# Optimization experiments

Hardware: AMD Instinct MI355X
Metric: run time of the kernel (lower is better)

Reference implementation:

```python
import math
import jax, jax.numpy as jnp
import numpy as np

T_MIN = 0.1
T_MAX = 1.0


def _log_cond_prob(energy, text_mask, mel_mask, direction, neg):
    # energy: (B, I, J); returns (B, I, J, K) with K=J (alpha) or J-1 (beta)
    B, I, J = energy.shape
    if direction == 'alpha':
        K = J
        tri_jk = jnp.arange(J)[:, None] >= jnp.arange(K)[None, :]  # torch triu: valid if j >= k
    else:
        K = J - 1
        tri_jk = jnp.arange(J)[:, None] <= jnp.arange(K)[None, :]  # torch tril: valid if j <= k
    tm = text_mask[:, :, None, None]           # (B,I,1,1)
    mmj = mel_mask[:, None, :, None]           # (B,1,J,1)
    mmk = mel_mask[:, None, None, :K]          # (B,1,1,K)
    mask = tm & mmj & mmk                      # (B,I,J,K)
    tri = tri_jk[None, None] & mask
    mask_invalid = jnp.broadcast_to(tm & mmk, (B, I, J, K))
    text_invalid = jnp.broadcast_to(tm, (B, I, J, K))
    right_mask = mask | (~mask_invalid)
    e = jnp.broadcast_to(energy[..., None], (B, I, J, K))
    e = jnp.where((~tri) & mask_invalid, neg, e)
    e = jnp.where(~mask_invalid, -10.0, e)
    e = e - jax.nn.logsumexp(e, axis=2, keepdims=True)  # normalize over mel dim j
    e = jnp.where(~mask_invalid, neg, e)
    e = jnp.where(~right_mask, -10.0, e)
    e = jnp.where(~text_invalid, -10.0, e)
    return e


def _roll(x, shifts, axis):
    # per-batch roll of x along `axis` by shifts[b]
    return jax.vmap(lambda xb, s: jnp.roll(xb, s, axis=axis - 1))(x, shifts)


def _right_shift(x, sh_t, sh_m):
    x = _roll(x, sh_t, 1)
    x = _roll(x, sh_m, 2)
    return _roll(x, sh_m.at[1:].add(-1), 3)  # faithful to in-place shifts_mel_dim[1:] -= 1


def _left_shift(x, sh_t, sh_m):
    x = x[..., None]
    x = _roll(x, -sh_t, 1)
    x = _roll(x, -sh_m, 2)
    return x[..., 0]


def _compute_alpha(lcp_a, neg):
    # alpha[:, i, j] = lse_k(alpha[:, i-1, k] + lcp_a[:, i-1, j-1, k]) for j >= i
    B, I, J, _ = lcp_a.shape
    j_idx = jnp.arange(J + 1)
    row0 = jnp.full((B, J + 1), neg, dtype=lcp_a.dtype).at[:, 0].set(0.0)

    def step(prev, xs):  # prev = alpha[:, i-1, :J]
        lcp_i, i = xs
        new = jax.nn.logsumexp(prev[:, None, :] + lcp_i, axis=2)  # (B, J), index j-1
        row = jnp.concatenate([jnp.full((B, 1), neg, dtype=new.dtype), new], axis=1)
        row = jnp.where(j_idx[None, :] >= i, row, neg)
        return row[:, :J], row

    _, rows = jax.lax.scan(step, row0[:, :J], (jnp.swapaxes(lcp_a, 0, 1), jnp.arange(1, I + 1)))
    return jnp.concatenate([row0[:, None, :], jnp.swapaxes(rows, 0, 1)], axis=1)  # (B, I+1, J+1)


def _compute_beta(lcp_b, neg):
    # beta[:, i, j] = lse_k(beta[:, i+1, k+1] + lcp_b[:, i, j, k]) for j < J+i-I+1
    B, I, J, _ = lcp_b.shape
    j_idx = jnp.arange(J)
    last = jnp.full((B, J), neg, dtype=lcp_b.dtype).at[:, J - 1].set(0.0)

    def step(nxt, xs):
        lcp_i, i = xs
        full = jax.nn.logsumexp(nxt[:, 1:][:, None, :] + lcp_i, axis=2)  # (B, J)
        row = jnp.where(j_idx[None, :] < (J + i - I + 1), full, neg)
        return row, row

    _, rows = jax.lax.scan(step, last, (jnp.swapaxes(lcp_b[:, :I - 1], 0, 1), jnp.arange(I - 1)), reverse=True)
    return jnp.concatenate([jnp.swapaxes(rows, 0, 1), last[:, None, :]], axis=1)  # (B, I, J)


def _forward(text_embeddings, mel_embeddings, text_mask, mel_mask, noise, temperature_ratio, neg):
    B, I, Dt = text_embeddings.shape
    _, J, Dm = mel_embeddings.shape
    energy = jnp.einsum('bid,bjd->bij', text_embeddings, mel_embeddings) / math.sqrt(Dt * Dm)
    temp = T_MIN + (T_MAX - T_MIN) * temperature_ratio[0]
    energy = (energy - jnp.log(-jnp.log(noise))) / temp  # Gumbel noise + temperature
    lcp_a = _log_cond_prob(energy, text_mask, mel_mask, 'alpha', neg)
    alpha = _compute_alpha(lcp_a, neg)
    t_len = text_mask.sum(1)
    m_len = mel_mask.sum(1)
    sh_t = t_len.max() - t_len
    sh_m = m_len.max() - m_len
    lcp_b = _log_cond_prob(energy, text_mask, mel_mask, 'beta', neg)
    lcp_b = _right_shift(lcp_b, sh_t, sh_m)
    beta = _compute_beta(lcp_b, neg)
    beta = _left_shift(beta, sh_t, sh_m)
    gamma = alpha[:, 1:, 1:] + beta
    gamma_mask = text_mask[:, :, None] & mel_mask[:, None, :]
    gls_mask = jnp.broadcast_to(text_mask[:, :, None], (B, I, J)) | gamma_mask
    gamma = jnp.where(gls_mask, gamma, neg)
    gamma = gamma - jax.nn.logsumexp(gamma, axis=1, keepdims=True)  # normalize over text dim
    gamma = jnp.where(gamma_mask, gamma, neg)
    expanded = jnp.einsum('bij,bid->bjd', jnp.exp(gamma), text_embeddings)
    expanded = expanded * mel_mask[:, :, None]
    return gamma, expanded


def setup_inputs() -> dict:
    key = jax.random.key(0)
    k1, k2, k3, k4 = jax.random.split(key, 4)
    B, I, J, Dt, Dm = 1, 128, 640, 256, 256
    text_embeddings = jax.random.normal(k1, (B, I, Dt), dtype=jnp.float32)
    mel_embeddings = jax.random.normal(k2, (B, J, Dm), dtype=jnp.float32)
    text_mask = jnp.ones((B, I), dtype=bool)
    mel_mask = jnp.ones((B, J), dtype=bool)
    noise = jnp.clip(jax.random.uniform(k3, (B, I, J), dtype=jnp.float32), 1e-8, 1.0 - 1e-8)
    temperature_ratio = jax.random.uniform(k4, (1,), dtype=jnp.float32)
    return {
        'text_embeddings': text_embeddings,
        'mel_embeddings': mel_embeddings,
        'text_mask': text_mask,
        'mel_mask': mel_mask,
        'noise': noise,
        'temperature_ratio': temperature_ratio,
    }


def reference(text_embeddings, mel_embeddings, text_mask, mel_mask, noise, temperature_ratio):
    return _forward(text_embeddings, mel_embeddings, text_mask, mel_mask, noise, temperature_ratio, -jnp.inf)
```

## Files before the change

### kernel.cpp

```cpp
#include <hip/hip_runtime.h>
#include <math.h>

constexpr int TI = 128;
constexpr int TJ = 640;
constexpr int TD = 256;
constexpr int EPL = 10;
constexpr int NS  = 3;
constexpr int CH  = 4;
constexpr int NP  = 6;

#define NEG (-1e30f)
#define LOG2E 1.44269504088896340736f
#define LN2   0.69314718055994530942f

__device__ __forceinline__ float rexp2(float x) { return __builtin_amdgcn_exp2f(x); }
__device__ __forceinline__ float rlog2(float x) { return __builtin_amdgcn_logf(x); }

struct MS { float m, s; };
__device__ __forceinline__ MS ms_combine(MS a, MS b) {
    float d = b.m - a.m;
    bool al = d <= 0.0f;
    float m = al ? a.m : b.m;
    float t = rexp2(al ? d : -d);
    float s = al ? fmaf(b.s, t, a.s) : fmaf(a.s, t, b.s);
    return {m, s};
}
__device__ __forceinline__ MS ms_push(MS run, float x) { return ms_combine(run, {x, 1.0f}); }
__device__ __forceinline__ float ms_final(MS a) {
    return (a.m < -1e29f) ? NEG : a.m + rlog2(a.s);
}

template<int CTRL, int RMASK>
__device__ __forceinline__ float dpp_f(float src, float oldv) {
    int r = __builtin_amdgcn_update_dpp(
        __float_as_int(oldv), __float_as_int(src), CTRL, RMASK, 0xF, false);
    return __int_as_float(r);
}
template<int CTRL, int RMASK>
__device__ __forceinline__ MS dpp_ms(MS v) {
    MS t;
    t.m = dpp_f<CTRL, RMASK>(v.m, NEG);
    t.s = dpp_f<CTRL, RMASK>(v.s, 0.0f);
    return t;
}
__device__ __forceinline__ MS wave_incl_scan_ms(MS v) {
    v = ms_combine(dpp_ms<0x111, 0xF>(v), v);
    v = ms_combine(dpp_ms<0x112, 0xF>(v), v);
    v = ms_combine(dpp_ms<0x114, 0xF>(v), v);
    v = ms_combine(dpp_ms<0x118, 0xF>(v), v);
    v = ms_combine(dpp_ms<0x142, 0xA>(v), v);
    v = ms_combine(dpp_ms<0x143, 0xC>(v), v);
    return v;
}
__device__ __forceinline__ MS wave_excl_from_incl_ms(MS incl) {
    return dpp_ms<0x138, 0xF>(incl);
}
__device__ __forceinline__ float wave_incl_scan_add(float v) {
    v += dpp_f<0x111, 0xF>(v, 0.0f);
    v += dpp_f<0x112, 0xF>(v, 0.0f);
    v += dpp_f<0x114, 0xF>(v, 0.0f);
    v += dpp_f<0x118, 0xF>(v, 0.0f);
    v += dpp_f<0x142, 0xA>(v, 0.0f);
    v += dpp_f<0x143, 0xC>(v, 0.0f);
    return v;
}
__device__ __forceinline__ float wave_incl_scan_max(float v) {
    v = fmaxf(v, dpp_f<0x111, 0xF>(v, NEG));
    v = fmaxf(v, dpp_f<0x112, 0xF>(v, NEG));
    v = fmaxf(v, dpp_f<0x114, 0xF>(v, NEG));
    v = fmaxf(v, dpp_f<0x118, 0xF>(v, NEG));
    v = fmaxf(v, dpp_f<0x142, 0xA>(v, NEG));
    v = fmaxf(v, dpp_f<0x143, 0xC>(v, NEG));
    return v;
}
__device__ __forceinline__ float readlane63(float v) {
    return __int_as_float(__builtin_amdgcn_readlane(__float_as_int(v), 63));
}
__device__ __forceinline__ float readlaneN(float v, int n) {
    return __int_as_float(__builtin_amdgcn_readlane(__float_as_int(v), n));
}

__device__ __forceinline__ void cbar() { asm volatile("" ::: "memory"); }
__device__ __forceinline__ int opaque_zero(int v) {
    int r;
    asm("v_xor_b32 %0, %1, %1" : "=v"(r) : "v"(v));
    return r;
}
__device__ __forceinline__ int pollwait(volatile int* flag, int need) {
    int rv;
    do { rv = *flag; } while (rv < need);
    return rv;
}

__device__ __forceinline__ void load10(float* d, const float* s) {
    const float2* p = (const float2*)s;
    #pragma unroll
    for (int k = 0; k < 5; k++) { float2 v = p[k]; d[2*k] = v.x; d[2*k+1] = v.y; }
}
__device__ __forceinline__ void store10(float* d, const float* v) {
    float2* p = (float2*)d;
    #pragma unroll
    for (int k = 0; k < 5; k++) { float2 t; t.x = v[2*k]; t.y = v[2*k+1]; p[k] = t; }
}

__global__ __launch_bounds__(256) void k_melT(
        const float* __restrict__ mel, float* __restrict__ melT) {
    __shared__ float ldsT[64][65];
    int j0 = blockIdx.x * 64, c0 = blockIdx.y * 64, tid = threadIdx.x;
    int rr = tid >> 4, c4 = tid & 15;
    #pragma unroll
    for (int p = 0; p < 4; p++) {
        int r = p * 16 + rr;
        float4 v = *(const float4*)(mel + (size_t)(j0 + r) * TD + c0 + c4 * 4);
        ldsT[c4 * 4 + 0][r] = v.x;
        ldsT[c4 * 4 + 1][r] = v.y;
        ldsT[c4 * 4 + 2][r] = v.z;
        ldsT[c4 * 4 + 3][r] = v.w;
    }
    __syncthreads();
    int jj = tid & 63, cw = tid >> 6;
    #pragma unroll
    for (int p = 0; p < 16; p++) {
        int cc = p * 4 + cw;
        melT[(size_t)(c0 + cc) * TJ + j0 + jj] = ldsT[cc][jj];
    }
}

__global__ __launch_bounds__(640) void k_energy(
        const float* __restrict__ text, const float* __restrict__ melT,
        const float* __restrict__ noise, const float* __restrict__ trat,
        float* __restrict__ energy, float* __restrict__ Ga,
        float* __restrict__ Gb, float* __restrict__ Cst) {
    __shared__ float trowm[TD], trowc[TD], trowp[TD];
    __shared__ float erowm[TJ], erowc[TJ], erowp[TJ];
    __shared__ float pcur[TJ], scur[TJ];
    __shared__ float wred[2][EPL];
    int i = blockIdx.x, tid = threadIdx.x;
    if (tid < TD) {
        trowc[tid] = text[i * TD + tid];
        trowm[tid] = (i > 0)      ? text[(i - 1) * TD + tid] : 0.0f;
        trowp[tid] = (i < TI - 1) ? text[(i + 1) * TD + tid] : 0.0f;
    }
    __syncthreads();
    float temp = 0.1f + 0.9f * trat[0];
    float sc = LOG2E / temp;
    int j = tid;
    float am = 0.0f, ac = 0.0f, ap = 0.0f;
    #pragma unroll 8
    for (int c = 0; c < TD; c++) {
        float m = melT[(size_t)c * TJ + j];
        am = fmaf(trowm[c], m, am);
        ac = fmaf(trowc[c], m, ac);
        ap = fmaf(trowp[c], m, ap);
    }
    float gm = (i > 0)      ? logf(-logf(noise[(i - 1) * TJ + j])) : 0.0f;
    float gc =                logf(-logf(noise[i * TJ + j]));
    float gp = (i < TI - 1) ? logf(-logf(noise[(i + 1) * TJ + j])) : 0.0f;
    erowm[j] = (am * (1.0f / 256.0f) - gm) * sc;
    float e2 = (ac * (1.0f / 256.0f) - gc) * sc;
    erowc[j] = e2;
    erowp[j] = (ap * (1.0f / 256.0f) - gp) * sc;
    energy[i * TJ + j] = e2;
    __syncthreads();
    if (tid < 64) {
        int l = tid;
        MS loc = {NEG, 0.0f};
        #pragma unroll
        for (int q = 0; q < EPL; q++) loc = ms_push(loc, erowc[l * EPL + q]);
        MS off = wave_excl_from_incl_ms(wave_incl_scan_ms(loc));
        MS run = off;
        #pragma unroll
        for (int q = 0; q < EPL; q++) {
            run = ms_push(run, erowc[l * EPL + q]);
            pcur[l * EPL + q] = ms_final(run);
        }
        loc = {NEG, 0.0f};
        #pragma unroll
        for (int q = 0; q < EPL; q++) loc = ms_push(loc, erowc[TJ - 1 - (l * EPL + q)]);
        off = wave_excl_from_incl_ms(wave_incl_scan_ms(loc));
        run = off;
        #pragma unroll
        for (int q = 0; q < EPL; q++) {
            int idx = TJ - 1 - (l * EPL + q);
            run = ms_push(run, erowc[idx]);
            scur[idx] = ms_final(run);
        }
    }
    __syncthreads();
    float ga, gb;
    if (i == 0) ga = (j == 0) ? -scur[0] : NEG;
    else        ga = (j == 0) ? NEG : erowm[j - 1] - scur[j];
    bool has_b = (i <= TI - 2);
    if (has_b) {
        if (i == TI - 2) gb = (j == 1) ? -pcur[TJ - 2] : NEG;
        else             gb = (j == 0) ? NEG : erowp[TJ - j] - pcur[TJ - 1 - j];
    } else gb = NEG;
    int wv = tid >> 6, l = tid & 63;
    float ma = readlane63(wave_incl_scan_max(ga));
    float mb = readlane63(wave_incl_scan_max(gb));
    if (l == 0) { wred[0][wv] = ma; wred[1][wv] = mb; }
    __syncthreads();
    float Ca = wred[0][0], Cb = wred[1][0];
    #pragma unroll
    for (int k = 1; k < EPL; k++) {
        Ca = fmaxf(Ca, wred[0][k]);
        Cb = fmaxf(Cb, wred[1][k]);
    }
    Ga[i * TJ + j] = rexp2(ga - Ca);
    if (has_b) Gb[i * TJ + j] = rexp2(gb - Cb);
    if (tid == 0) { Cst[i] = Ca; if (has_b) Cst[TI + i] = Cb; }
}

__global__ __launch_bounds__(320, 1) void k_scan(
        const float* __restrict__ energy, const float* __restrict__ Ga,
        const float* __restrict__ Gb, const float* __restrict__ Cst,
        float* __restrict__ a, float* __restrict__ b) {
    __shared__ float Gring[NS][CH][TJ];
    __shared__ float Ppring[NP][TJ + 8];
    __shared__ int ready[NS];
    __shared__ int prow, cdone, ocnt[2];
    const int tid = threadIdx.x, wave = tid >> 6, l = tid & 63;
    const bool is_alpha = (blockIdx.x == 0);
    const int nrows = is_alpha ? TI : TI - 1;
    const int nch = (nrows + CH - 1) / CH;
    if (tid < NS) ready[tid] = 0;
    if (tid == 0) { prow = 0; cdone = 0; ocnt[0] = 0; ocnt[1] = 0; }
    __syncthreads();

    if (wave == 0) {
        float C0, C1;
        if (is_alpha) { C0 = Cst[l]; C1 = Cst[64 + l]; }
        else          { C0 = Cst[128 + l]; C1 = Cst[192 + l]; }
        float Pp[EPL];
        #pragma unroll
        for (int q = 0; q < EPL; q++) Pp[q] = 0.0f;
        float rprev = 0.0f, Lam = 0.0f;
        int seen0 = 0, seen1 = 0;
        for (int c = 0; c < nch; c++) {
            int rv = pollwait(&ready[c % NS], c + 1);
            cbar();
            int tok = opaque_zero(rv);
            float Gr[CH][EPL];
            #pragma unroll
            for (int q = 0; q < CH; q++)
                if (c * CH + q < nrows)
                    load10(Gr[q], &Gring[c % NS][q][l * EPL + tok]);
            #pragma unroll
            for (int s = 0; s < CH; s++) {
                int t = c * CH + s;
                if (t < nrows) {
                    float lp[EPL];
                    if (t == 0) {
                        #pragma unroll
                        for (int q = 0; q < EPL; q++) lp[q] = Gr[0][q];
                    } else {
                        float carry = dpp_f<0x138, 0xF>(Pp[EPL - 1], 0.0f);
                        float rp = rprev;
                        lp[0] = carry * rp * Gr[s][0];
                        #pragma unroll
                        for (int q = 1; q < EPL; q++) lp[q] = Pp[q - 1] * rp * Gr[s][q];
                    }
                    #pragma unroll
                    for (int q = 9; q >= 1; q--) lp[q] += lp[q - 1];
                    #pragma unroll
                    for (int q = 9; q >= 2; q--) lp[q] += lp[q - 2];
                    #pragma unroll
                    for (int q = 9; q >= 4; q--) lp[q] += lp[q - 4];
                    #pragma unroll
                    for (int q = 9; q >= 8; q--) lp[q] += lp[q - 8];
                    float incl = wave_incl_scan_add(lp[EPL - 1]);
                    float excl = dpp_f<0x138, 0xF>(incl, 0.0f);
                    #pragma unroll
                    for (int q = 0; q < EPL; q++) Pp[q] = excl + lp[q];
                    float T = readlane63(incl);
                    int idx2 = is_alpha ? t : (126 - t);
                    float Cc = (idx2 < 64) ? readlaneN(C0, idx2) : readlaneN(C1, idx2 - 64);
                    float basev = Lam + Cc;
                    if (t >= NP) {
                        int need = ((t - NP) >> 1) + 1;
                        if (t & 1) {
                            if (seen1 < need) { seen1 = pollwait(&ocnt[1], need); cbar(); }
                        } else {
                            if (seen0 < need) { seen0 = pollwait(&ocnt[0], need); cbar(); }
                        }
                    }
                    int ps = t % NP;
                    store10(&Ppring[ps][l * EPL], Pp);
                    if (l == 0) Ppring[ps][TJ] = basev;
                    cbar();
                    if (l == 0) *(volatile int*)&prow = t + 1;
                    Lam = basev + rlog2(T);
                    rprev = (T > 0.0f) ? __builtin_amdgcn_rcpf(T) : 0.0f;
                }
            }
            cbar();
            if (l == 0) *(volatile int*)&cdone = c + 1;
        }
    } else if (wave <= 2) {
        const float* Gsrc = is_alpha ? Ga : Gb;
        for (int c = wave - 1; c < nch; c += 2) {
            if (c >= NS) { int dv = pollwait(&cdone, c - NS + 1); cbar(); (void)dv; }
            int slot = c % NS;
            int cnt = nrows - c * CH; if (cnt > CH) cnt = CH;
            int m0 = is_alpha ? c * CH : (TI - 2 - c * CH - (cnt - 1));
            const float4* src = (const float4*)(Gsrc + (size_t)m0 * TJ);
            int total4 = cnt * (TJ / 4);
            #pragma unroll
            for (int it = 0; it < CH * TJ / 4 / 64; it++) {
                int o4 = it * 64 + l;
                if (o4 < total4) {
                    float4 v = src[o4];
                    int ri = o4 / 160, c4 = o4 - ri * 160;
                    int s = is_alpha ? ri : (cnt - 1 - ri);
                    ((float4*)Gring[slot][s])[c4] = v;
                }
            }
            __threadfence_block();
            if (l == 0) *(volatile int*)&ready[slot] = c + 1;
        }
    } else {
        int w = wave - 3;
        if (!is_alpha && w == 0) {
            #pragma unroll
            for (int k = 0; k < EPL; k++) {
                int j = l + 64 * k;
                b[(TI - 1) * TJ + j] = (j == TJ - 1) ? 0.0f : NEG;
            }
        }
        for (int t = w; t < nrows; t += 2) {
            int row = is_alpha ? t : (TI - 2 - t);
            const float* Erow = energy + (size_t)row * TJ;
            float ev[EPL];
            #pragma unroll
            for (int k = 0; k < EPL; k++) ev[k] = Erow[l + 64 * k];
            int rv = pollwait(&prow, t + 1);
            cbar();
            int tok = opaque_zero(rv);
            int ps = t % NP;
            float base = Ppring[ps][TJ + tok];
            float ov[EPL];
            #pragma unroll
            for (int k = 0; k < EPL; k++) {
                int j = l + 64 * k;
                int pj = is_alpha ? j : (TJ - 1 - j);
                ov[k] = ev[k] + rlog2(Ppring[ps][pj + tok]) + base;
            }
            float* dst = (is_alpha ? a : b) + (size_t)row * TJ;
            #pragma unroll
            for (int k = 0; k < EPL; k++) dst[l + 64 * k] = ov[k];
            cbar();
            if (l == 0) *(volatile int*)&ocnt[w] = (t >> 1) + 1;
        }
    }
}

__global__ __launch_bounds__(256) void k_gamma(
        const float* __restrict__ a, const float* __restrict__ b,
        const float* __restrict__ text,
        float* __restrict__ outg, float* __restrict__ oute) {
    __shared__ float w128[TI];
    __shared__ float redm[2], reds[2];
    int j = blockIdx.x, tid = threadIdx.x;
    float gg = NEG;
    if (tid < TI) {
        float av = a[tid * TJ + j];
        float bv = b[tid * TJ + j];
        gg = (av < -1e29f || bv < -1e29f) ? NEG : av + bv;
        MS v = {gg, 1.0f};
        #pragma unroll
        for (int off = 32; off > 0; off >>= 1) {
            float om = __shfl_xor(v.m, off, 64);
            float os = __shfl_xor(v.s, off, 64);
            v = ms_combine(v, {om, os});
        }
        if ((tid & 63) == 0) { redm[tid >> 6] = v.m; reds[tid >> 6] = v.s; }
    }
    __syncthreads();
    float lse = ms_final(ms_combine({redm[0], reds[0]}, {redm[1], reds[1]}));
    if (tid < TI) {
        bool fin = gg > -1e29f;
        outg[tid * TJ + j] = fin ? (gg - lse) * LN2 : NEG;
        w128[tid] = fin ? rexp2(gg - lse) : 0.0f;
    }
    __syncthreads();
    float acc = 0.0f;
    #pragma unroll 8
    for (int ii = 0; ii < TI; ii++) acc += w128[ii] * text[ii * TD + tid];
    oute[(size_t)j * TD + tid] = acc;
}

extern "C" void kernel_launch(void* const* d_in, const int* in_sizes, int n_in,
                              void* d_out, int out_size, void* d_ws, size_t ws_size,
                              hipStream_t stream) {
    const float* text  = (const float*)d_in[0];
    const float* mel   = (const float*)d_in[1];
    const float* noise = (const float*)d_in[4];
    const float* trat  = (const float*)d_in[5];

    float* outg = (float*)d_out;
    float* oute = outg + TI * TJ;

    float* w      = (float*)d_ws;
    float* energy = w;
    float* Ga     = w + 1 * TI * TJ;
    float* Gb     = w + 2 * TI * TJ;
    float* Cst    = Gb + (size_t)(TI - 1) * TJ;
    float* melT   = w + 3 * TI * TJ;
    float* aArr   = w + 3 * TI * TJ;
    float* bArr   = w + 4 * TI * TJ;

    k_melT  <<<dim3(TJ / 64, TD / 64), 256, 0, stream>>>(mel, melT);
    k_energy<<<TI, TJ, 0, stream>>>(text, melT, noise, trat, energy, Ga, Gb, Cst);
    k_scan  <<<2, 320, 0, stream>>>(energy, Ga, Gb, Cst, aArr, bArr);
    k_gamma <<<TJ, 256, 0, stream>>>(aArr, bArr, text, outg, oute);
}
```

Baseline: 146.2 us.

## Deepen scan pipeline rings and use four output waves with energy prefetch

Doubles the G staging ring and the prefix-product ring depth, and raises the scan block from 5 to 7 waves so four output waves (instead of two) each handle every fourth row. Output waves now prefetch the next energy row while waiting for the scan wave. The producer's backpressure check is rewritten per chunk slot. The goal is to keep the serial scan wave from stalling on output writers or loads, at the cost of more LDS and more waves polling shared flags.

Result: no change. 144.4 us (-1.2%).

```diff
diff --git a/kernel.cpp b/kernel.cpp
--- a/kernel.cpp
+++ b/kernel.cpp
@@ -5,9 +5,10 @@
 constexpr int TJ = 640;
 constexpr int TD = 256;
 constexpr int EPL = 10;
-constexpr int NS  = 3;
+constexpr int NS  = 6;
 constexpr int CH  = 4;
-constexpr int NP  = 6;
+constexpr int NP  = 12;
+constexpr int NPC = NP / CH;
 
 #define NEG (-1e30f)
 #define LOG2E 1.44269504088896340736f
@@ -211,20 +212,20 @@
     if (tid == 0) { Cst[i] = Ca; if (has_b) Cst[TI + i] = Cb; }
 }
 
-__global__ __launch_bounds__(320, 1) void k_scan(
+__global__ __launch_bounds__(448, 1) void k_scan(
         const float* __restrict__ energy, const float* __restrict__ Ga,
         const float* __restrict__ Gb, const float* __restrict__ Cst,
         float* __restrict__ a, float* __restrict__ b) {
     __shared__ float Gring[NS][CH][TJ];
     __shared__ float Ppring[NP][TJ + 8];
     __shared__ int ready[NS];
-    __shared__ int prow, cdone, ocnt[2];
+    __shared__ int prow, cdone, ocnt[4];
     const int tid = threadIdx.x, wave = tid >> 6, l = tid & 63;
     const bool is_alpha = (blockIdx.x == 0);
     const int nrows = is_alpha ? TI : TI - 1;
     const int nch = (nrows + CH - 1) / CH;
     if (tid < NS) ready[tid] = 0;
-    if (tid == 0) { prow = 0; cdone = 0; ocnt[0] = 0; ocnt[1] = 0; }
+    if (tid == 0) { prow = 0; cdone = 0; ocnt[0] = 0; ocnt[1] = 0; ocnt[2] = 0; ocnt[3] = 0; }
     __syncthreads();
 
     if (wave == 0) {
@@ -235,7 +236,7 @@
         #pragma unroll
         for (int q = 0; q < EPL; q++) Pp[q] = 0.0f;
         float rprev = 0.0f, Lam = 0.0f;
-        int seen0 = 0, seen1 = 0;
+        int seen0 = 0, seen1 = 0, seen2 = 0, seen3 = 0;
         for (int c = 0; c < nch; c++) {
             int rv = pollwait(&ready[c % NS], c + 1);
             cbar();
@@ -276,13 +277,12 @@
                     int idx2 = is_alpha ? t : (126 - t);
                     float Cc = (idx2 < 64) ? readlaneN(C0, idx2) : readlaneN(C1, idx2 - 64);
                     float basev = Lam + Cc;
-                    if (t >= NP) {
-                        int need = ((t - NP) >> 1) + 1;
-                        if (t & 1) {
-                            if (seen1 < need) { seen1 = pollwait(&ocnt[1], need); cbar(); }
-                        } else {
-                            if (seen0 < need) { seen0 = pollwait(&ocnt[0], need); cbar(); }
-                        }
+                    if (c >= NPC) {
+                        int need = c - NPC + 1;
+                        if (s == 0)      { if (seen0 < need) { seen0 = pollwait(&ocnt[0], need); cbar(); } }
+                        else if (s == 1) { if (seen1 < need) { seen1 = pollwait(&ocnt[1], need); cbar(); } }
+                        else if (s == 2) { if (seen2 < need) { seen2 = pollwait(&ocnt[2], need); cbar(); } }
+                        else             { if (seen3 < need) { seen3 = pollwait(&ocnt[3], need); cbar(); } }
                     }
                     int ps = t % NP;
                     store10(&Ppring[ps][l * EPL], Pp);
@@ -327,12 +327,22 @@
                 b[(TI - 1) * TJ + j] = (j == TJ - 1) ? 0.0f : NEG;
             }
         }
-        for (int t = w; t < nrows; t += 2) {
-            int row = is_alpha ? t : (TI - 2 - t);
-            const float* Erow = energy + (size_t)row * TJ;
-            float ev[EPL];
+        float* dst_arr = is_alpha ? a : b;
+        float ev[EPL], evn[EPL];
+        {
+            int row0 = is_alpha ? w : (TI - 2 - w);
+            const float* Erow = energy + (size_t)row0 * TJ;
             #pragma unroll
             for (int k = 0; k < EPL; k++) ev[k] = Erow[l + 64 * k];
+        }
+        for (int t = w; t < nrows; t += 4) {
+            int tn = t + 4;
+            if (tn < nrows) {
+                int rown = is_alpha ? tn : (TI - 2 - tn);
+                const float* Erown = energy + (size_t)rown * TJ;
+                #pragma unroll
+                for (int k = 0; k < EPL; k++) evn[k] = Erown[l + 64 * k];
+            }
             int rv = pollwait(&prow, t + 1);
             cbar();
             int tok = opaque_zero(rv);
@@ -345,11 +355,14 @@
                 int pj = is_alpha ? j : (TJ - 1 - j);
                 ov[k] = ev[k] + rlog2(Ppring[ps][pj + tok]) + base;
             }
-            float* dst = (is_alpha ? a : b) + (size_t)row * TJ;
+            int row = is_alpha ? t : (TI - 2 - t);
+            float* dst = dst_arr + (size_t)row * TJ;
             #pragma unroll
             for (int k = 0; k < EPL; k++) dst[l + 64 * k] = ov[k];
             cbar();
-            if (l == 0) *(volatile int*)&ocnt[w] = (t >> 1) + 1;
+            if (l == 0) *(volatile int*)&ocnt[w] = ((t - w) >> 2) + 1;
+            #pragma unroll
+            for (int k = 0; k < EPL; k++) ev[k] = evn[k];
         }
     }
 }
@@ -411,6 +424,6 @@
 
     k_melT  <<<dim3(TJ / 64, TD / 64), 256, 0, stream>>>(mel, melT);
     k_energy<<<TI, TJ, 0, stream>>>(text, melT, noise, trat, energy, Ga, Gb, Cst);
-    k_scan  <<<2, 320, 0, stream>>>(energy, Ga, Gb, Cst, aArr, bArr);
+    k_scan  <<<2, 448, 0, stream>>>(energy, Ga, Gb, Cst, aArr, bArr);
     k_gamma <<<TJ, 256, 0, stream>>>(aArr, bArr, text, outg, oute);
 }
```

## Replace warp-specialized LDS pipeline in scan with single-wave register prefetch

Applied to the files above, without the earlier changes.

The scan kernel used five waves: one doing the recurrence, two loader waves staging G rows into LDS rings, and two output waves computing log outputs, all coordinated through LDS flag polling. Now a single wave per block does everything. It prefetches G and energy rows into registers four rows ahead and writes each output row directly from its own Pp registers. This removes LDS round-trips and spin-wait synchronization from the serial critical path, but puts the log/output work and global loads back onto the one sequential wave.

Result: slower. 158.7 us (+8.5%).

```diff
diff --git a/kernel.cpp b/kernel.cpp
--- a/kernel.cpp
+++ b/kernel.cpp
@@ -5,9 +5,6 @@
 constexpr int TJ = 640;
 constexpr int TD = 256;
 constexpr int EPL = 10;
-constexpr int NS  = 3;
-constexpr int CH  = 4;
-constexpr int NP  = 6;
 
 #define NEG (-1e30f)
 #define LOG2E 1.44269504088896340736f
@@ -78,18 +75,6 @@
 }
 __device__ __forceinline__ float readlaneN(float v, int n) {
     return __int_as_float(__builtin_amdgcn_readlane(__float_as_int(v), n));
-}
-
-__device__ __forceinline__ void cbar() { asm volatile("" ::: "memory"); }
-__device__ __forceinline__ int opaque_zero(int v) {
-    int r;
-    asm("v_xor_b32 %0, %1, %1" : "=v"(r) : "v"(v));
-    return r;
-}
-__device__ __forceinline__ int pollwait(volatile int* flag, int need) {
-    int rv;
-    do { rv = *flag; } while (rv < need);
-    return rv;
 }
 
 __device__ __forceinline__ void load10(float* d, const float* s) {
@@ -211,145 +196,103 @@
     if (tid == 0) { Cst[i] = Ca; if (has_b) Cst[TI + i] = Cb; }
 }
 
-__global__ __launch_bounds__(320, 1) void k_scan(
+__global__ __launch_bounds__(64, 1) void k_scan(
         const float* __restrict__ energy, const float* __restrict__ Ga,
         const float* __restrict__ Gb, const float* __restrict__ Cst,
         float* __restrict__ a, float* __restrict__ b) {
-    __shared__ float Gring[NS][CH][TJ];
-    __shared__ float Ppring[NP][TJ + 8];
-    __shared__ int ready[NS];
-    __shared__ int prow, cdone, ocnt[2];
-    const int tid = threadIdx.x, wave = tid >> 6, l = tid & 63;
+    constexpr int PF = 4;
+    const int l = threadIdx.x;
     const bool is_alpha = (blockIdx.x == 0);
     const int nrows = is_alpha ? TI : TI - 1;
-    const int nch = (nrows + CH - 1) / CH;
-    if (tid < NS) ready[tid] = 0;
-    if (tid == 0) { prow = 0; cdone = 0; ocnt[0] = 0; ocnt[1] = 0; }
-    __syncthreads();
-
-    if (wave == 0) {
-        float C0, C1;
-        if (is_alpha) { C0 = Cst[l]; C1 = Cst[64 + l]; }
-        else          { C0 = Cst[128 + l]; C1 = Cst[192 + l]; }
-        float Pp[EPL];
-        #pragma unroll
-        for (int q = 0; q < EPL; q++) Pp[q] = 0.0f;
-        float rprev = 0.0f, Lam = 0.0f;
-        int seen0 = 0, seen1 = 0;
-        for (int c = 0; c < nch; c++) {
-            int rv = pollwait(&ready[c % NS], c + 1);
-            cbar();
-            int tok = opaque_zero(rv);
-            float Gr[CH][EPL];
-            #pragma unroll
-            for (int q = 0; q < CH; q++)
-                if (c * CH + q < nrows)
-                    load10(Gr[q], &Gring[c % NS][q][l * EPL + tok]);
-            #pragma unroll
-            for (int s = 0; s < CH; s++) {
-                int t = c * CH + s;
-                if (t < nrows) {
-                    float lp[EPL];
-                    if (t == 0) {
-                        #pragma unroll
-                        for (int q = 0; q < EPL; q++) lp[q] = Gr[0][q];
-                    } else {
-                        float carry = dpp_f<0x138, 0xF>(Pp[EPL - 1], 0.0f);
-                        float rp = rprev;
-                        lp[0] = carry * rp * Gr[s][0];
-                        #pragma unroll
-                        for (int q = 1; q < EPL; q++) lp[q] = Pp[q - 1] * rp * Gr[s][q];
-                    }
+    const float* Gsrc = is_alpha ? Ga : Gb;
+    float* dst_arr = is_alpha ? a : b;
+    const int eoff = is_alpha ? (l * EPL) : ((63 - l) * EPL);
+
+    float C0, C1;
+    if (is_alpha) { C0 = Cst[l];       C1 = Cst[64 + l]; }
+    else          { C0 = Cst[128 + l]; C1 = Cst[192 + l]; }
+
+    if (!is_alpha) {
+        float init[EPL];
+        #pragma unroll
+        for (int q = 0; q < EPL; q++) {
+            int j = l * EPL + q;
+            init[q] = (j == TJ - 1) ? 0.0f : NEG;
+        }
+        store10(&b[(size_t)(TI - 1) * TJ + l * EPL], init);
+    }
+
+    float g[PF][EPL], e[PF][EPL];
+    #pragma unroll
+    for (int s = 0; s < PF; s++) {
+        if (s < nrows) {
+            int row = is_alpha ? s : (TI - 2 - s);
+            load10(g[s], Gsrc + (size_t)row * TJ + l * EPL);
+            load10(e[s], energy + (size_t)row * TJ + eoff);
+        }
+    }
+
+    float Pp[EPL];
+    #pragma unroll
+    for (int q = 0; q < EPL; q++) Pp[q] = 0.0f;
+    float rprev = 0.0f, Lam = 0.0f;
+
+    for (int tb = 0; tb < TI; tb += PF) {
+        #pragma unroll
+        for (int s = 0; s < PF; s++) {
+            int t = tb + s;
+            if (t < nrows) {
+                float lp[EPL];
+                if (t == 0) {
                     #pragma unroll
-                    for (int q = 9; q >= 1; q--) lp[q] += lp[q - 1];
+                    for (int q = 0; q < EPL; q++) lp[q] = g[s][q];
+                } else {
+                    float carry = dpp_f<0x138, 0xF>(Pp[EPL - 1], 0.0f);
+                    float rp = rprev;
+                    lp[0] = carry * rp * g[s][0];
                     #pragma unroll
-                    for (int q = 9; q >= 2; q--) lp[q] += lp[q - 2];
+                    for (int q = 1; q < EPL; q++) lp[q] = Pp[q - 1] * rp * g[s][q];
+                }
+                #pragma unroll
+                for (int q = 9; q >= 1; q--) lp[q] += lp[q - 1];
+                #pragma unroll
+                for (int q = 9; q >= 2; q--) lp[q] += lp[q - 2];
+                #pragma unroll
+                for (int q = 9; q >= 4; q--) lp[q] += lp[q - 4];
+                #pragma unroll
+                for (int q = 9; q >= 8; q--) lp[q] += lp[q - 8];
+                float incl = wave_incl_scan_add(lp[EPL - 1]);
+                float excl = dpp_f<0x138, 0xF>(incl, 0.0f);
+                #pragma unroll
+                for (int q = 0; q < EPL; q++) Pp[q] = excl + lp[q];
+                float T = readlane63(incl);
+                int idx2 = is_alpha ? t : (126 - t);
+                float Cc = (idx2 < 64) ? readlaneN(C0, idx2) : readlaneN(C1, idx2 - 64);
+                float basev = Lam + Cc;
+
+                int row = is_alpha ? t : (TI - 2 - t);
+                float ov[EPL];
+                if (is_alpha) {
                     #pragma unroll
-                    for (int q = 9; q >= 4; q--) lp[q] += lp[q - 4];
+                    for (int q = 0; q < EPL; q++)
+                        ov[q] = e[s][q] + rlog2(Pp[q]) + basev;
+                } else {
                     #pragma unroll
-                    for (int q = 9; q >= 8; q--) lp[q] += lp[q - 8];
-                    float incl = wave_incl_scan_add(lp[EPL - 1]);
-                    float excl = dpp_f<0x138, 0xF>(incl, 0.0f);
-                    #pragma unroll
-                    for (int q = 0; q < EPL; q++) Pp[q] = excl + lp[q];
-                    float T = readlane63(incl);
-                    int idx2 = is_alpha ? t : (126 - t);
-                    float Cc = (idx2 < 64) ? readlaneN(C0, idx2) : readlaneN(C1, idx2 - 64);
-                    float basev = Lam + Cc;
-                    if (t >= NP) {
-                        int need = ((t - NP) >> 1) + 1;
-                        if (t & 1) {
-                            if (seen1 < need) { seen1 = pollwait(&ocnt[1], need); cbar(); }
-                        } else {
-                            if (seen0 < need) { seen0 = pollwait(&ocnt[0], need); cbar(); }
-                        }
-                    }
-                    int ps = t % NP;
-                    store10(&Ppring[ps][l * EPL], Pp);
-                    if (l == 0) Ppring[ps][TJ] = basev;
-                    cbar();
-                    if (l == 0) *(volatile int*)&prow = t + 1;
-                    Lam = basev + rlog2(T);
-                    rprev = (T > 0.0f) ? __builtin_amdgcn_rcpf(T) : 0.0f;
+                    for (int m = 0; m < EPL; m++)
+                        ov[m] = e[s][m] + rlog2(Pp[9 - m]) + basev;
+                }
+                store10(dst_arr + (size_t)row * TJ + eoff, ov);
+
+                Lam = basev + rlog2(T);
+                rprev = (T > 0.0f) ? __builtin_amdgcn_rcpf(T) : 0.0f;
+
+                int tp = t + PF;
+                if (tp < nrows) {
+                    int rowp = is_alpha ? tp : (TI - 2 - tp);
+                    load10(g[s], Gsrc + (size_t)rowp * TJ + l * EPL);
+                    load10(e[s], energy + (size_t)rowp * TJ + eoff);
                 }
             }
-            cbar();
-            if (l == 0) *(volatile int*)&cdone = c + 1;
-        }
-    } else if (wave <= 2) {
-        const float* Gsrc = is_alpha ? Ga : Gb;
-        for (int c = wave - 1; c < nch; c += 2) {
-            if (c >= NS) { int dv = pollwait(&cdone, c - NS + 1); cbar(); (void)dv; }
-            int slot = c % NS;
-            int cnt = nrows - c * CH; if (cnt > CH) cnt = CH;
-            int m0 = is_alpha ? c * CH : (TI - 2 - c * CH - (cnt - 1));
-            const float4* src = (const float4*)(Gsrc + (size_t)m0 * TJ);
-            int total4 = cnt * (TJ / 4);
-            #pragma unroll
-            for (int it = 0; it < CH * TJ / 4 / 64; it++) {
-                int o4 = it * 64 + l;
-                if (o4 < total4) {
-                    float4 v = src[o4];
-                    int ri = o4 / 160, c4 = o4 - ri * 160;
-                    int s = is_alpha ? ri : (cnt - 1 - ri);
-                    ((float4*)Gring[slot][s])[c4] = v;
-                }
-            }
-            __threadfence_block();
-            if (l == 0) *(volatile int*)&ready[slot] = c + 1;
-        }
-    } else {
-        int w = wave - 3;
-        if (!is_alpha && w == 0) {
-            #pragma unroll
-            for (int k = 0; k < EPL; k++) {
-                int j = l + 64 * k;
-                b[(TI - 1) * TJ + j] = (j == TJ - 1) ? 0.0f : NEG;
-            }
-        }
-        for (int t = w; t < nrows; t += 2) {
-            int row = is_alpha ? t : (TI - 2 - t);
-            const float* Erow = energy + (size_t)row * TJ;
-            float ev[EPL];
-            #pragma unroll
-            for (int k = 0; k < EPL; k++) ev[k] = Erow[l + 64 * k];
-            int rv = pollwait(&prow, t + 1);
-            cbar();
-            int tok = opaque_zero(rv);
-            int ps = t % NP;
-            float base = Ppring[ps][TJ + tok];
-            float ov[EPL];
-            #pragma unroll
-            for (int k = 0; k < EPL; k++) {
-                int j = l + 64 * k;
-                int pj = is_alpha ? j : (TJ - 1 - j);
-                ov[k] = ev[k] + rlog2(Ppring[ps][pj + tok]) + base;
-            }
-            float* dst = (is_alpha ? a : b) + (size_t)row * TJ;
-            #pragma unroll
-            for (int k = 0; k < EPL; k++) dst[l + 64 * k] = ov[k];
-            cbar();
-            if (l == 0) *(volatile int*)&ocnt[w] = (t >> 1) + 1;
         }
     }
 }
@@ -411,6 +354,6 @@
 
     k_melT  <<<dim3(TJ / 64, TD / 64), 256, 0, stream>>>(mel, melT);
     k_energy<<<TI, TJ, 0, stream>>>(text, melT, noise, trat, energy, Ga, Gb, Cst);
-    k_scan  <<<2, 320, 0, stream>>>(energy, Ga, Gb, Cst, aArr, bArr);
+    k_scan  <<<2, 64, 0, stream>>>(energy, Ga, Gb, Cst, aArr, bArr);
     k_gamma <<<TJ, 256, 0, stream>>>(aArr, bArr, text, outg, oute);
 }
```
